# Optimization experiments

Hardware: AMD Instinct MI355X
Metric: run time of the kernel (lower is better)

The kernel has to match this reference:

```python
import jax, jax.numpy as jnp
import numpy as np

B, L, D, H = 16, 1024, 128, 256


def setup_inputs() -> dict:
    key = jax.random.key(0)
    ks = jax.random.split(key, 32)
    inp = {
        "x": jax.random.normal(ks[0], (B, L, D), jnp.float32),
        "y": jax.random.normal(ks[1], (B, L, D), jnp.float32),
        "z": jax.random.normal(ks[2], (B, L, D), jnp.float32),
        "len_x": jax.random.randint(ks[3], (B,), L // 2, L + 1, dtype=jnp.int32),
        "len_y": jax.random.randint(ks[4], (B,), L // 2, L + 1, dtype=jnp.int32),
        "len_z": jax.random.randint(ks[5], (B,), L // 2, L + 1, dtype=jnp.int32),
    }
    s1 = (2.0 / (D + H)) ** 0.5  # xavier-normal for first layer
    s2 = (2.0 / (H + D)) ** 0.5
    i = 6
    for name in ("W1", "B1", "W2", "B2"):
        inp[f"{name}_l1_w"] = jax.random.normal(ks[i + 0], (D, H), jnp.float32) * s1
        inp[f"{name}_l1_b"] = jnp.zeros((H,), jnp.float32)
        inp[f"{name}_l2_w"] = jax.random.normal(ks[i + 1], (H, D), jnp.float32) * s2
        inp[f"{name}_l2_b"] = jnp.zeros((D,), jnp.float32)
        i += 2
    return inp


def _mlp(c, w1, b1, w2, b2):
    h = jax.nn.gelu(c @ w1 + b1, approximate=False)  # torch nn.GELU = exact erf form
    return h @ w2 + b2


def _batched_ragged_dft(xc, lengths, inverse):
    # Per-sample DFT over the first lengths[i] timesteps; rows/cols >= l are zero.
    _, Ls, _ = xc.shape
    t = jnp.arange(Ls, dtype=jnp.int32)
    kt = t[:, None] * t[None, :]                      # [L,L] integer k*t
    l = lengths[:, None, None]                        # [B,1,1]
    ktm = kt[None, :, :] % l                          # exact phase reduction mod l
    sign = 1.0 if inverse else -1.0
    phase = sign * 2.0 * jnp.pi * ktm.astype(jnp.float32) / l.astype(jnp.float32)
    mask = (t[None, :, None] < l) & (t[None, None, :] < l)
    E = jnp.where(mask, jnp.exp(1j * phase).astype(jnp.complex64), 0.0)
    if inverse:
        E = E / l.astype(jnp.complex64)
    return jnp.einsum("bkt,btd->bkd", E, xc)


def _complex_relu(f):
    # torch: where(|z|>0, |z|*exp(i*angle(z)), 0)
    mag = jnp.abs(f)
    safe = jnp.where(mag > 0, f, jnp.asarray(1.0 + 0.0j, jnp.complex64))
    act = jnp.abs(safe) * jnp.exp(1j * jnp.angle(safe))
    return jnp.where(mag > 0, act.astype(jnp.complex64), 0.0)


def reference(x, y, z, len_x, len_y, len_z,
              W1_l1_w, W1_l1_b, W1_l2_w, W1_l2_b,
              B1_l1_w, B1_l1_b, B1_l2_w, B1_l2_b,
              W2_l1_w, W2_l1_b, W2_l2_w, W2_l2_b,
              B2_l1_w, B2_l1_b, B2_l2_w, B2_l2_b):
    x_freq = _batched_ragged_dft(x.astype(jnp.complex64), len_x, inverse=False)
    c1 = jnp.sum(y, axis=1) / len_y[:, None].astype(jnp.float32)
    c2 = jnp.sum(z, axis=1) / len_z[:, None].astype(jnp.float32)
    W1 = _mlp(c1, W1_l1_w, W1_l1_b, W1_l2_w, W1_l2_b).astype(jnp.complex64)
    b1 = _mlp(c1, B1_l1_w, B1_l1_b, B1_l2_w, B1_l2_b).astype(jnp.complex64)
    W2 = _mlp(c2, W2_l1_w, W2_l1_b, W2_l2_w, W2_l2_b).astype(jnp.complex64)
    b2 = _mlp(c2, B2_l1_w, B2_l1_b, B2_l2_w, B2_l2_b).astype(jnp.complex64)
    filtered = x_freq * (1.0 + (W1 + W2)[:, None, :] / 2.0) + (b1 + b2)[:, None, :] / 2.0
    activated = _complex_relu(filtered)
    x_recon = _batched_ragged_dft(activated, len_x, inverse=True)
    return x_recon.real
```

## Files before the change

### kernel.cpp

```cpp
#include <hip/hip_runtime.h>
#include <math.h>

constexpr int NB = 16;
constexpr int SL = 1024;
constexpr int ND = 128;
constexpr int NH = 256;
constexpr int NSTILE = 18;
constexpr int NKTILE = 17;
constexpr int EPAD = 584;

constexpr size_t PLANE_S = (size_t)NB * 8 * NSTILE * 1024;
constexpr size_t PLANE_K = (size_t)NB * 8 * NKTILE * 1024;
constexpr size_t CS_OFF = 0;
constexpr size_t DD_OFF = PLANE_S;
constexpr size_t FR_OFF = 2 * PLANE_S;
constexpr size_t FI_OFF = 2 * PLANE_S + PLANE_K;
constexpr size_t F32B      = PLANE_S + PLANE_K;
constexpr size_t P_OFF     = F32B;
constexpr size_t SCALE_OFF = P_OFF + 2 * 16 * 16 * 128;
constexpr size_t BIAS_OFF  = SCALE_OFF + NB * ND;

typedef float          f32x4 __attribute__((ext_vector_type(4)));
typedef unsigned int   u32x4 __attribute__((ext_vector_type(4)));
typedef unsigned short u16x8 __attribute__((ext_vector_type(8)));

__device__ __forceinline__ unsigned short f2bf(float f) {
    unsigned u = __float_as_uint(f);
    return (unsigned short)((u + 0x7FFFu + ((u >> 16) & 1u)) >> 16);
}
__device__ __forceinline__ float hw_sin(float rev) {
    float r; asm("v_sin_f32 %0, %1" : "=v"(r) : "v"(rev)); return r;
}
__device__ __forceinline__ float hw_cos(float rev) {
    float r; asm("v_cos_f32 %0, %1" : "=v"(r) : "v"(rev)); return r;
}
__device__ __forceinline__ void mfma16(f32x4& acc, u32x4 a, u32x4 b) {
    asm("v_mfma_f32_16x16x32_bf16 %0, %1, %2, %0" : "+v"(acc) : "v"(a), "v"(b));
}
__device__ __forceinline__ float4 f4add(float4 a, float4 b) {
    return make_float4(a.x + b.x, a.y + b.y, a.z + b.z, a.w + b.w);
}

__global__ __launch_bounds__(256) void k_front(const float* __restrict__ x,
                                               const float* __restrict__ y,
                                               const float* __restrict__ z,
                                               const int* __restrict__ len_x,
                                               float* __restrict__ wsf,
                                               unsigned short* __restrict__ wsb,
                                               float* __restrict__ out) {
    const int blk = blockIdx.x;
    const int tid = threadIdx.x;
    __shared__ float4 red4[256];

    if (blk < 512) {
        const int ch  = blk & 15;
        const int b   = (blk >> 4) & 15;
        const int src = blk >> 8;
        const float* base = (src == 0 ? y : z) + ((size_t)b * SL + ch * 64) * ND;
        const int dg = tid & 31;
        const int tq = tid >> 5;
        float4 s = make_float4(0.f, 0.f, 0.f, 0.f);
#pragma unroll
        for (int j = 0; j < 8; ++j)
            s = f4add(s, *(const float4*)&base[(size_t)(tq + 8 * j) * ND + dg * 4]);
        red4[tid] = s;
        __syncthreads();
        if (tq < 4) red4[tid] = f4add(red4[tid], red4[tid + 128]);
        __syncthreads();
        if (tq < 2) red4[tid] = f4add(red4[tid], red4[tid + 64]);
        __syncthreads();
        if (tq == 0) {
            const float4 r = f4add(red4[dg], red4[dg + 32]);
            *(float4*)&wsf[P_OFF + ((size_t)((src * NB + b) * 16 + ch)) * ND + dg * 4] = r;
        }
        return;
    }

    if (blk < 800) {
        const int pb = blk - 512;
        const int bx = pb % NSTILE;
        const int b  = pb / NSTILE;
        const int l = len_x[b];
        const int NS = (l >> 1) + 1;
        const int d = tid & 127;
        const int slot = tid >> 7;
        const int dblk = d >> 4, dw = d & 15;
#pragma unroll
        for (int it = 0; it < 2; ++it) {
            const int sb = (bx * 4 + slot * 2 + it) * 8;
            u16x8 cb, db;
#pragma unroll
            for (int j = 0; j < 8; ++j) {
                const int s = sb + j;
                float c = 0.f, dd = 0.f;
                if (s < NS) {
                    const float a = x[((size_t)b * SL + s) * ND + d];
                    float p = 0.f;
                    if (s > 0 && 2 * s != l) p = x[((size_t)b * SL + (l - s)) * ND + d];
                    c = a + p; dd = a - p;
                }
                cb[j] = f2bf(c); db[j] = f2bf(dd);
            }
            const int sg = (sb >> 3) & 3;
            const size_t ro = ((size_t)((b * 8 + dblk) * NSTILE) + bx) * 1024 + sg * 128 + dw * 8;
            *(u16x8*)&wsb[CS_OFF + ro] = cb;
            *(u16x8*)&wsb[DD_OFF + ro] = db;
            if (sb + 7 >= NS && sb < NKTILE * 32) {
                const u16x8 zz = {0, 0, 0, 0, 0, 0, 0, 0};
                const size_t ko = ((size_t)((b * 8 + dblk) * NKTILE) + (sb >> 5)) * 1024 + sg * 128 + dw * 8;
                *(u16x8*)&wsb[FR_OFF + ko] = zz;
                *(u16x8*)&wsb[FI_OFF + ko] = zz;
            }
        }
        return;
    }

    {
        const int zb = blk - 800;
        const int b = zb >> 3;
        const int seg = zb & 7;
        const int l = len_x[b];
        const int row = 512 + seg * 64 + (tid >> 2);
        if (row >= l) {
            const int c16 = (tid & 3) * 32;
            float* p = &out[((size_t)b * SL + row) * ND + c16];
            const float4 zz = make_float4(0.f, 0.f, 0.f, 0.f);
#pragma unroll
            for (int q = 0; q < 8; ++q)
                *(float4*)&p[q * 4] = zz;
        }
        return;
    }
}

__global__ __launch_bounds__(256) void k_fwd_mlp(
    const int* __restrict__ len_x,
    const int* __restrict__ len_y, const int* __restrict__ len_z,
    float* __restrict__ wsf, unsigned short* __restrict__ wsb,
    const float* __restrict__ W1w1, const float* __restrict__ W1b1,
    const float* __restrict__ W1w2, const float* __restrict__ W1b2,
    const float* __restrict__ B1w1, const float* __restrict__ B1b1,
    const float* __restrict__ B1w2, const float* __restrict__ B1b2,
    const float* __restrict__ W2w1, const float* __restrict__ W2b1,
    const float* __restrict__ W2w2, const float* __restrict__ W2b2,
    const float* __restrict__ B2w1, const float* __restrict__ B2b1,
    const float* __restrict__ B2w2, const float* __restrict__ B2b2) {
    const int tid = threadIdx.x;

    if (blockIdx.x >= 528) {
        const int mb = blockIdx.x - 528;
        const int pair = mb & 1;
        const int b    = mb >> 1;

        const float* w1a = pair ? B1w1 : W1w1;  const float* b1a = pair ? B1b1 : W1b1;
        const float* w2a = pair ? B1w2 : W1w2;  const float* b2a = pair ? B1b2 : W1b2;
        const float* w1b = pair ? B2w1 : W2w1;  const float* b1b = pair ? B2b1 : W2b1;
        const float* w2b = pair ? B2w2 : W2w2;  const float* b2b = pair ? B2b2 : W2b2;

        __shared__ float c1s[ND], c2s[ND];
        __shared__ float h0[NH], h1[NH];
        __shared__ float oa[ND], ob[ND];

        if (tid < ND) {
            float s = 0.f;
            for (int ch = 0; ch < 16; ++ch)
                s += wsf[P_OFF + ((size_t)((0 * NB + b) * 16 + ch)) * ND + tid];
            c1s[tid] = s / (float)len_y[b];
        } else {
            const int d = tid - ND;
            float s = 0.f;
            for (int ch = 0; ch < 16; ++ch)
                s += wsf[P_OFF + ((size_t)((1 * NB + b) * 16 + ch)) * ND + d];
            c2s[d] = s / (float)len_z[b];
        }
        __syncthreads();

        {
            const int j = tid;
            float s0 = b1a[j], s1 = b1b[j];
            for (int i = 0; i < ND; ++i) {
                s0 = fmaf(c1s[i], w1a[i * NH + j], s0);
                s1 = fmaf(c2s[i], w1b[i * NH + j], s1);
            }
            h0[j] = 0.5f * s0 * (1.f + erff(s0 * 0.7071067811865475f));
            h1[j] = 0.5f * s1 * (1.f + erff(s1 * 0.7071067811865475f));
        }
        __syncthreads();

        {
            const bool second = tid >= ND;
            const int d = second ? tid - ND : tid;
            const float* w = second ? w2b : w2a;
            const float* hh = second ? h1 : h0;
            float s = second ? b2b[d] : b2a[d];
            for (int j = 0; j < NH; ++j)
                s = fmaf(hh[j], w[j * ND + d], s);
            if (second) ob[d] = s; else oa[d] = s;
        }
        __syncthreads();

        if (tid < ND) {
            if (pair == 0)
                wsf[SCALE_OFF + b * ND + tid] = 1.f + 0.5f * (oa[tid] + ob[tid]);
            else
                wsf[BIAS_OFF  + b * ND + tid] = 0.5f * (oa[tid] + ob[tid]);
        }
        return;
    }

    const int bid = blockIdx.x;
    const int b7 = bid & 7;
    const int q  = bid >> 3;
    const int b  = (q / 33) * 8 + b7;
    const int kbase = (q % 33) * 16;

    const int l = len_x[b];
    const int NS = (l >> 1) + 1;
    if (kbase >= NS) return;
    const float invl = 1.f / (float)l;
    const float fl = (float)l;

    __shared__ __align__(16) unsigned short Ec[16][EPAD];
    __shared__ __align__(16) unsigned short Es[16][EPAD];

    const int lane = tid & 63, wave = tid >> 6;
    const int lrow = lane & 15, lkg = lane >> 4;

    {
        const int row = tid >> 4;
        const int colbase = (tid & 15) * 36;
        const int kk = kbase + row;
#pragma unroll 6
        for (int j = 0; j < 36; j += 2) {
            unsigned cw = 0, sw = 0;
#pragma unroll
            for (int h = 0; h < 2; ++h) {
                const int sg = colbase + j + h;
                float cv = 0.f, sv = 0.f;
                if (sg < NS) {
                    const float ks = (float)(kk * sg);
                    float idxf = fmaf(-fl, floorf(ks * invl), ks);
                    idxf = (idxf < 0.f) ? idxf + fl : idxf;
                    const float rev = idxf * invl;
                    cv = hw_cos(rev);
                    sv = -hw_sin(rev);
                }
                cw |= (unsigned)f2bf(cv) << (16 * h);
                sw |= (unsigned)f2bf(sv) << (16 * h);
            }
            *(unsigned*)&Ec[row][colbase + j] = cw;
            *(unsigned*)&Es[row][colbase + j] = sw;
        }
    }
    __syncthreads();

    f32x4 accR[2], accI[2];
#pragma unroll
    for (int t = 0; t < 2; ++t) { accR[t] = 0.f; accI[t] = 0.f; }

    const size_t tb0 = ((size_t)((b * 8 + 2 * wave + 0) * NSTILE)) * 1024 + lane * 8;
    const size_t tb1 = ((size_t)((b * 8 + 2 * wave + 1) * NSTILE)) * 1024 + lane * 8;

    for (int s0 = 0; s0 < NS; s0 += 32) {
        const int stile = s0 >> 5;
        const u32x4 eC = *(const u32x4*)&Ec[lrow][s0 + lkg * 8];
        const u32x4 eS = *(const u32x4*)&Es[lrow][s0 + lkg * 8];
        const u32x4 aC0 = *(const u32x4*)&wsb[CS_OFF + tb0 + (size_t)stile * 1024];
        const u32x4 aD0 = *(const u32x4*)&wsb[DD_OFF + tb0 + (size_t)stile * 1024];
        const u32x4 aC1 = *(const u32x4*)&wsb[CS_OFF + tb1 + (size_t)stile * 1024];
        const u32x4 aD1 = *(const u32x4*)&wsb[DD_OFF + tb1 + (size_t)stile * 1024];
        mfma16(accR[0], aC0, eC);
        mfma16(accI[0], aD0, eS);
        mfma16(accR[1], aC1, eC);
        mfma16(accI[1], aD1, eS);
    }

    unsigned short (*FRst)[16] = (unsigned short(*)[16])&Ec[0][0];
    unsigned short (*FIst)[16] = (unsigned short(*)[16])&Es[0][0];

    __syncthreads();
    {
        const int kcol = kbase + lrow;
        const float w = ((kcol == 0 || 2 * kcol == l) ? 1.f : 2.f) * invl;
#pragma unroll
        for (int t = 0; t < 2; ++t) {
#pragma unroll
            for (int r = 0; r < 4; ++r) {
                const int drow = wave * 32 + t * 16 + lkg * 4 + r;
                FRst[drow][lrow] = f2bf(w * accR[t][r]);
                FIst[drow][lrow] = f2bf(w * accI[t][r]);
            }
        }
    }
    __syncthreads();

    {
        const int dblk = tid >> 5;
        const int kgi  = (tid >> 4) & 1;
        const int dw   = tid & 15;
        const int ktile = kbase >> 5;
        const int kg0 = (kbase & 16) ? 2 : 0;
        const size_t go = ((size_t)((b * 8 + dblk) * NKTILE) + ktile) * 1024
                        + (kg0 + kgi) * 128 + dw * 8;
        const int d = dblk * 16 + dw;
        if (kbase + 15 < NS) {
            *(u16x8*)&wsb[FR_OFF + go] = *(u16x8*)&FRst[d][kgi * 8];
            *(u16x8*)&wsb[FI_OFF + go] = *(u16x8*)&FIst[d][kgi * 8];
        } else {
            u16x8 fr, fi;
#pragma unroll
            for (int e = 0; e < 8; ++e) {
                const int kc = kbase + kgi * 8 + e;
                fr[e] = (kc < NS) ? FRst[d][kgi * 8 + e] : (unsigned short)0;
                fi[e] = (kc < NS) ? FIst[d][kgi * 8 + e] : (unsigned short)0;
            }
            *(u16x8*)&wsb[FR_OFF + go] = fr;
            *(u16x8*)&wsb[FI_OFF + go] = fi;
        }
    }
}

__global__ __launch_bounds__(256) void k_inv(const int* __restrict__ len_x,
                                             const float* __restrict__ wsf,
                                             const unsigned short* __restrict__ wsb,
                                             float* __restrict__ out) {
    const int bid = blockIdx.x;
    const int b7 = bid & 7;
    const int q  = bid >> 3;
    const int b  = (q / 33) * 8 + b7;
    const int tbase = (q % 33) * 16;

    const int l = len_x[b];
    const int NS = (l >> 1) + 1;
    if (tbase >= NS) return;
    const float invl = 1.f / (float)l;
    const float fl = (float)l;

    __shared__ __align__(16) unsigned short E2c[16][EPAD];
    __shared__ __align__(16) unsigned short E2s[16][EPAD];

    const int tid = threadIdx.x;
    const int lane = tid & 63, wave = tid >> 6;
    const int lrow = lane & 15, lkg = lane >> 4;

    {
        const int row = tid >> 4;
        const int colbase = (tid & 15) * 36;
        const int tt = tbase + row;
#pragma unroll 6
        for (int j = 0; j < 36; j += 2) {
            unsigned cw = 0, sw = 0;
#pragma unroll
            for (int h = 0; h < 2; ++h) {
                const int kg = colbase + j + h;
                float cv = 0.f, sv = 0.f;
                if (kg < NS) {
                    const float tk = (float)(tt * kg);
                    float idxf = fmaf(-fl, floorf(tk * invl), tk);
                    idxf = (idxf < 0.f) ? idxf + fl : idxf;
                    const float rev = idxf * invl;
                    cv = hw_cos(rev);
                    sv = hw_sin(rev);
                }
                cw |= (unsigned)f2bf(cv) << (16 * h);
                sw |= (unsigned)f2bf(sv) << (16 * h);
            }
            *(unsigned*)&E2c[row][colbase + j] = cw;
            *(unsigned*)&E2s[row][colbase + j] = sw;
        }
    }
    __syncthreads();

    const int dc0 = wave * 32 + lrow;
    const int dc1 = wave * 32 + 16 + lrow;
    const float sc0 = wsf[SCALE_OFF + b * ND + dc0];
    const float sc1 = wsf[SCALE_OFF + b * ND + dc1];
    const float bi0 = wsf[BIAS_OFF + b * ND + dc0];
    const float bi1 = wsf[BIAS_OFF + b * ND + dc1];

    f32x4 accA[2], accB[2];
#pragma unroll
    for (int t = 0; t < 2; ++t) { accA[t] = 0.f; accB[t] = 0.f; }

    const size_t tb0 = ((size_t)((b * 8 + 2 * wave + 0) * NKTILE)) * 1024 + lane * 8;
    const size_t tb1 = ((size_t)((b * 8 + 2 * wave + 1) * NKTILE)) * 1024 + lane * 8;

    for (int k0 = 0; k0 < NS; k0 += 32) {
        const int ktile = k0 >> 5;
        const u32x4 aC = *(const u32x4*)&E2c[lrow][k0 + lkg * 8];
        const u32x4 aS = *(const u32x4*)&E2s[lrow][k0 + lkg * 8];
        const u32x4 bR0 = *(const u32x4*)&wsb[FR_OFF + tb0 + (size_t)ktile * 1024];
        const u32x4 bI0 = *(const u32x4*)&wsb[FI_OFF + tb0 + (size_t)ktile * 1024];
        const u32x4 bR1 = *(const u32x4*)&wsb[FR_OFF + tb1 + (size_t)ktile * 1024];
        const u32x4 bI1 = *(const u32x4*)&wsb[FI_OFF + tb1 + (size_t)ktile * 1024];
        mfma16(accA[0], aC, bR0);
        mfma16(accB[0], aS, bI0);
        mfma16(accA[1], aC, bR1);
        mfma16(accB[1], aS, bI1);
    }

    float (*O1)[ND] = (float(*)[ND])&E2c[0][0];
    float (*O2)[ND] = (float(*)[ND])&E2s[0][0];

    __syncthreads();
#pragma unroll
    for (int t = 0; t < 2; ++t) {
        const int dcol = (t == 0) ? dc0 : dc1;
        const float sc = (t == 0) ? sc0 : sc1;
        const float bi = (t == 0) ? bi0 : bi1;
#pragma unroll
        for (int r = 0; r < 4; ++r) {
            const int ro = lkg * 4 + r;
            const float vA = accA[t][r], vB = accB[t][r];
            float va = (vA - vB) * sc;
            if (tbase + ro == 0) va += bi;
            O1[ro][dcol] = va;
            O2[ro][dcol] = (vA + vB) * sc;
        }
    }
    __syncthreads();

    {
        const int r8 = tid >> 4;
        const int c8 = (tid & 15) * 8;
        const int trow = tbase + r8;
        if (trow < NS) {
            float* p = &out[((size_t)b * SL + trow) * ND + c8];
            *(float4*)p = *(float4*)&O1[r8][c8];
            *(float4*)(p + 4) = *(float4*)&O1[r8][c8 + 4];
            if (trow > 0 && 2 * trow != l) {
                float* q2 = &out[((size_t)b * SL + (l - trow)) * ND + c8];
                *(float4*)q2 = *(float4*)&O2[r8][c8];
                *(float4*)(q2 + 4) = *(float4*)&O2[r8][c8 + 4];
            }
        }
    }
}

extern "C" void kernel_launch(void* const* d_in, const int* in_sizes, int n_in,
                              void* d_out, int out_size, void* d_ws, size_t ws_size,
                              hipStream_t stream) {
    const float* x = (const float*)d_in[0];
    const float* y = (const float*)d_in[1];
    const float* z = (const float*)d_in[2];
    const int* len_x = (const int*)d_in[3];
    const int* len_y = (const int*)d_in[4];
    const int* len_z = (const int*)d_in[5];
    float* wsf = (float*)d_ws;
    unsigned short* wsb = (unsigned short*)d_ws;
    float* out = (float*)d_out;

    k_front<<<928, 256, 0, stream>>>(x, y, z, len_x, wsf, wsb, out);

    k_fwd_mlp<<<560, 256, 0, stream>>>(len_x, len_y, len_z, wsf, wsb,
        (const float*)d_in[6],  (const float*)d_in[7],  (const float*)d_in[8],  (const float*)d_in[9],
        (const float*)d_in[10], (const float*)d_in[11], (const float*)d_in[12], (const float*)d_in[13],
        (const float*)d_in[14], (const float*)d_in[15], (const float*)d_in[16], (const float*)d_in[17],
        (const float*)d_in[18], (const float*)d_in[19], (const float*)d_in[20], (const float*)d_in[21]);

    k_inv<<<528, 256, 0, stream>>>(len_x, wsf, wsb, out);
}
```

Measured before the change: 46.23 us.

## Split DFT reduction dimension across two wave groups with LDS partial-sum merge

Doubles the block size of the forward and inverse DFT kernels to 512 threads. The extra four waves take the second half of the reduction tiles and write their partial accumulators to shared memory, and the first half adds them in before the epilogue. The goal is more latency hiding and more in-flight global loads per block on the MFMA loop. The cost is an extra LDS round trip and barrier, plus idle threads in the table-build and store phases.

```diff
diff --git a/kernel.cpp b/kernel.cpp
--- a/kernel.cpp
+++ b/kernel.cpp
@@ -133,7 +133,7 @@
     }
 }
 
-__global__ __launch_bounds__(256) void k_fwd_mlp(
+__global__ __launch_bounds__(512) void k_fwd_mlp(
     const int* __restrict__ len_x,
     const int* __restrict__ len_y, const int* __restrict__ len_z,
     float* __restrict__ wsf, unsigned short* __restrict__ wsb,
@@ -166,7 +166,7 @@
             for (int ch = 0; ch < 16; ++ch)
                 s += wsf[P_OFF + ((size_t)((0 * NB + b) * 16 + ch)) * ND + tid];
             c1s[tid] = s / (float)len_y[b];
-        } else {
+        } else if (tid < 256) {
             const int d = tid - ND;
             float s = 0.f;
             for (int ch = 0; ch < 16; ++ch)
@@ -175,7 +175,7 @@
         }
         __syncthreads();
 
-        {
+        if (tid < 256) {
             const int j = tid;
             float s0 = b1a[j], s1 = b1b[j];
             for (int i = 0; i < ND; ++i) {
@@ -187,7 +187,7 @@
         }
         __syncthreads();
 
-        {
+        if (tid < 256) {
             const bool second = tid >= ND;
             const int d = second ? tid - ND : tid;
             const float* w = second ? w2b : w2a;
@@ -223,10 +223,13 @@
     __shared__ __align__(16) unsigned short Ec[16][EPAD];
     __shared__ __align__(16) unsigned short Es[16][EPAD];
 
-    const int lane = tid & 63, wave = tid >> 6;
+    const int lane = tid & 63;
+    const int wave8 = tid >> 6;
+    const int shalf = wave8 >> 2;
+    const int w4    = wave8 & 3;
     const int lrow = lane & 15, lkg = lane >> 4;
 
-    {
+    if (tid < 256) {
         const int row = tid >> 4;
         const int colbase = (tid & 15) * 36;
         const int kk = kbase + row;
@@ -258,11 +261,16 @@
 #pragma unroll
     for (int t = 0; t < 2; ++t) { accR[t] = 0.f; accI[t] = 0.f; }
 
-    const size_t tb0 = ((size_t)((b * 8 + 2 * wave + 0) * NSTILE)) * 1024 + lane * 8;
-    const size_t tb1 = ((size_t)((b * 8 + 2 * wave + 1) * NSTILE)) * 1024 + lane * 8;
-
-    for (int s0 = 0; s0 < NS; s0 += 32) {
-        const int stile = s0 >> 5;
+    const size_t tb0 = ((size_t)((b * 8 + 2 * w4 + 0) * NSTILE)) * 1024 + lane * 8;
+    const size_t tb1 = ((size_t)((b * 8 + 2 * w4 + 1) * NSTILE)) * 1024 + lane * 8;
+
+    const int ntile = (NS + 31) >> 5;
+    const int mid = ntile >> 1;
+    const int st0 = shalf ? mid : 0;
+    const int st1 = shalf ? ntile : mid;
+
+    for (int stile = st0; stile < st1; ++stile) {
+        const int s0 = stile * 32;
         const u32x4 eC = *(const u32x4*)&Ec[lrow][s0 + lkg * 8];
         const u32x4 eS = *(const u32x4*)&Es[lrow][s0 + lkg * 8];
         const u32x4 aC0 = *(const u32x4*)&wsb[CS_OFF + tb0 + (size_t)stile * 1024];
@@ -275,26 +283,43 @@
         mfma16(accI[1], aD1, eS);
     }
 
+    float* PR = (float*)((char*)&Ec[0][0] + 4096);
+    float* PI = (float*)((char*)&Es[0][0] + 4096);
+
+    __syncthreads();
+    if (shalf == 1) {
+#pragma unroll
+        for (int t = 0; t < 2; ++t)
+#pragma unroll
+            for (int r = 0; r < 4; ++r) {
+                const int drow = w4 * 32 + t * 16 + lkg * 4 + r;
+                PR[drow * 16 + lrow] = accR[t][r];
+                PI[drow * 16 + lrow] = accI[t][r];
+            }
+    }
+    __syncthreads();
+
     unsigned short (*FRst)[16] = (unsigned short(*)[16])&Ec[0][0];
     unsigned short (*FIst)[16] = (unsigned short(*)[16])&Es[0][0];
 
-    __syncthreads();
-    {
+    if (shalf == 0) {
         const int kcol = kbase + lrow;
         const float w = ((kcol == 0 || 2 * kcol == l) ? 1.f : 2.f) * invl;
 #pragma unroll
         for (int t = 0; t < 2; ++t) {
 #pragma unroll
             for (int r = 0; r < 4; ++r) {
-                const int drow = wave * 32 + t * 16 + lkg * 4 + r;
-                FRst[drow][lrow] = f2bf(w * accR[t][r]);
-                FIst[drow][lrow] = f2bf(w * accI[t][r]);
-            }
-        }
-    }
-    __syncthreads();
-
-    {
+                const int drow = w4 * 32 + t * 16 + lkg * 4 + r;
+                const float vR = accR[t][r] + PR[drow * 16 + lrow];
+                const float vI = accI[t][r] + PI[drow * 16 + lrow];
+                FRst[drow][lrow] = f2bf(w * vR);
+                FIst[drow][lrow] = f2bf(w * vI);
+            }
+        }
+    }
+    __syncthreads();
+
+    if (tid < 256) {
         const int dblk = tid >> 5;
         const int kgi  = (tid >> 4) & 1;
         const int dw   = tid & 15;
@@ -320,7 +345,7 @@
     }
 }
 
-__global__ __launch_bounds__(256) void k_inv(const int* __restrict__ len_x,
+__global__ __launch_bounds__(512) void k_inv(const int* __restrict__ len_x,
                                              const float* __restrict__ wsf,
                                              const unsigned short* __restrict__ wsb,
                                              float* __restrict__ out) {
@@ -340,10 +365,13 @@
     __shared__ __align__(16) unsigned short E2s[16][EPAD];
 
     const int tid = threadIdx.x;
-    const int lane = tid & 63, wave = tid >> 6;
+    const int lane = tid & 63;
+    const int wave8 = tid >> 6;
+    const int shalf = wave8 >> 2;
+    const int w4    = wave8 & 3;
     const int lrow = lane & 15, lkg = lane >> 4;
 
-    {
+    if (tid < 256) {
         const int row = tid >> 4;
         const int colbase = (tid & 15) * 36;
         const int tt = tbase + row;
@@ -371,8 +399,8 @@
     }
     __syncthreads();
 
-    const int dc0 = wave * 32 + lrow;
-    const int dc1 = wave * 32 + 16 + lrow;
+    const int dc0 = w4 * 32 + lrow;
+    const int dc1 = w4 * 32 + 16 + lrow;
     const float sc0 = wsf[SCALE_OFF + b * ND + dc0];
     const float sc1 = wsf[SCALE_OFF + b * ND + dc1];
     const float bi0 = wsf[BIAS_OFF + b * ND + dc0];
@@ -382,11 +410,16 @@
 #pragma unroll
     for (int t = 0; t < 2; ++t) { accA[t] = 0.f; accB[t] = 0.f; }
 
-    const size_t tb0 = ((size_t)((b * 8 + 2 * wave + 0) * NKTILE)) * 1024 + lane * 8;
-    const size_t tb1 = ((size_t)((b * 8 + 2 * wave + 1) * NKTILE)) * 1024 + lane * 8;
-
-    for (int k0 = 0; k0 < NS; k0 += 32) {
-        const int ktile = k0 >> 5;
+    const size_t tb0 = ((size_t)((b * 8 + 2 * w4 + 0) * NKTILE)) * 1024 + lane * 8;
+    const size_t tb1 = ((size_t)((b * 8 + 2 * w4 + 1) * NKTILE)) * 1024 + lane * 8;
+
+    const int ntile = (NS + 31) >> 5;
+    const int mid = ntile >> 1;
+    const int kt0 = shalf ? mid : 0;
+    const int kt1 = shalf ? ntile : mid;
+
+    for (int ktile = kt0; ktile < kt1; ++ktile) {
+        const int k0 = ktile * 32;
         const u32x4 aC = *(const u32x4*)&E2c[lrow][k0 + lkg * 8];
         const u32x4 aS = *(const u32x4*)&E2s[lrow][k0 + lkg * 8];
         const u32x4 bR0 = *(const u32x4*)&wsb[FR_OFF + tb0 + (size_t)ktile * 1024];
@@ -399,28 +432,46 @@
         mfma16(accB[1], aS, bI1);
     }
 
+    float* PA = (float*)((char*)&E2c[0][0] + 8192);
+    float* PB = (float*)((char*)&E2s[0][0] + 8192);
+
+    __syncthreads();
+    if (shalf == 1) {
+#pragma unroll
+        for (int t = 0; t < 2; ++t)
+#pragma unroll
+            for (int r = 0; r < 4; ++r) {
+                const int dcol = w4 * 32 + t * 16 + lrow;
+                PA[dcol * 16 + lkg * 4 + r] = accA[t][r];
+                PB[dcol * 16 + lkg * 4 + r] = accB[t][r];
+            }
+    }
+    __syncthreads();
+
     float (*O1)[ND] = (float(*)[ND])&E2c[0][0];
     float (*O2)[ND] = (float(*)[ND])&E2s[0][0];
 
-    __syncthreads();
-#pragma unroll
-    for (int t = 0; t < 2; ++t) {
-        const int dcol = (t == 0) ? dc0 : dc1;
-        const float sc = (t == 0) ? sc0 : sc1;
-        const float bi = (t == 0) ? bi0 : bi1;
-#pragma unroll
-        for (int r = 0; r < 4; ++r) {
-            const int ro = lkg * 4 + r;
-            const float vA = accA[t][r], vB = accB[t][r];
-            float va = (vA - vB) * sc;
-            if (tbase + ro == 0) va += bi;
-            O1[ro][dcol] = va;
-            O2[ro][dcol] = (vA + vB) * sc;
-        }
-    }
-    __syncthreads();
-
-    {
+    if (shalf == 0) {
+#pragma unroll
+        for (int t = 0; t < 2; ++t) {
+            const int dcol = (t == 0) ? dc0 : dc1;
+            const float sc = (t == 0) ? sc0 : sc1;
+            const float bi = (t == 0) ? bi0 : bi1;
+#pragma unroll
+            for (int r = 0; r < 4; ++r) {
+                const int ro = lkg * 4 + r;
+                const float vA = accA[t][r] + PA[dcol * 16 + ro];
+                const float vB = accB[t][r] + PB[dcol * 16 + ro];
+                float va = (vA - vB) * sc;
+                if (tbase + ro == 0) va += bi;
+                O1[ro][dcol] = va;
+                O2[ro][dcol] = (vA + vB) * sc;
+            }
+        }
+    }
+    __syncthreads();
+
+    if (tid < 256) {
         const int r8 = tid >> 4;
         const int c8 = (tid & 15) * 8;
         const int trow = tbase + r8;
@@ -452,11 +503,11 @@
 
     k_front<<<928, 256, 0, stream>>>(x, y, z, len_x, wsf, wsb, out);
 
-    k_fwd_mlp<<<560, 256, 0, stream>>>(len_x, len_y, len_z, wsf, wsb,
+    k_fwd_mlp<<<560, 512, 0, stream>>>(len_x, len_y, len_z, wsf, wsb,
         (const float*)d_in[6],  (const float*)d_in[7],  (const float*)d_in[8],  (const float*)d_in[9],
         (const float*)d_in[10], (const float*)d_in[11], (const float*)d_in[12], (const float*)d_in[13],
         (const float*)d_in[14], (const float*)d_in[15], (const float*)d_in[16], (const float*)d_in[17],
         (const float*)d_in[18], (const float*)d_in[19], (const float*)d_in[20], (const float*)d_in[21]);
 
-    k_inv<<<528, 256, 0, stream>>>(len_x, wsf, wsb, out);
-}
+    k_inv<<<528, 512, 0, stream>>>(len_x, wsf, wsb, out);
+}
```

Result: no change. 46.66 us (+0.9%).
